# Performance work log

Hardware: AMD Instinct MI355X
Metric: run time of the kernel (lower is better)

## Reference

```python
import jax, jax.numpy as jnp
import numpy as np
from jax.scipy.linalg import solve_triangular

B, T, D = 4, 8192, 1024
HEAD_DIM = 128
CHUNK = 64


def setup_inputs() -> dict:
    key = jax.random.key(0)
    ks = jax.random.split(key, 8)
    H = D // HEAD_DIM
    x = jax.random.normal(ks[0], (B, T, D), dtype=jnp.float32)
    W_write = jax.random.normal(ks[1], (D, D), dtype=jnp.float32) * 0.02
    W_gate = jax.random.normal(ks[2], (H, D), dtype=jnp.float32) * 0.02
    W_out = jax.random.normal(ks[3], (D, D), dtype=jnp.float32) * 0.02
    W_beta = jax.random.normal(ks[4], (H, D), dtype=jnp.float32) * 0.02
    W_alpha = jax.random.normal(ks[5], (H, D), dtype=jnp.float32) * 0.02
    # dt_bias init as in torch: dt ~ loguniform(1e-3, 1e-1), bias = dt + log(-expm1(-dt))
    u = jax.random.uniform(ks[6], (H,), dtype=jnp.float32)
    dt = jnp.exp(u * (jnp.log(jnp.float32(0.1)) - jnp.log(jnp.float32(0.001))) + jnp.log(jnp.float32(0.001)))
    dt_bias = dt + jnp.log(-jnp.expm1(-dt))
    A_log = jnp.log(jax.random.uniform(ks[7], (H,), dtype=jnp.float32, minval=1e-3, maxval=16.0))
    return {"x": x, "W_write": W_write, "W_gate": W_gate, "W_out": W_out,
            "W_beta": W_beta, "W_alpha": W_alpha, "dt_bias": dt_bias, "A_log": A_log}


def reference(x, W_write, W_gate, W_out, W_beta, W_alpha, dt_bias, A_log):
    Bn, Tn, Dm = x.shape
    H = A_log.shape[0]
    d = Dm // H
    C = CHUNK
    assert Tn % C == 0
    N = Tn // C

    xf = x.astype(jnp.float32)
    v = (xf @ W_write.T).reshape(Bn, Tn, H, d)                       # write values
    gate = jax.nn.sigmoid(xf @ W_gate.T)[..., None]                  # (B,T,H,1)
    beta = jax.nn.sigmoid(xf @ W_beta.T)                             # (B,T,H)
    decay = -jnp.exp(A_log) * jax.nn.softplus(xf @ W_alpha.T + dt_bias)  # (B,T,H)

    rk = xf.reshape(Bn, Tn, H, d)
    rk = rk / jnp.maximum(jnp.linalg.norm(rk, axis=-1, keepdims=True), 1e-12)
    wk = jnp.pad(rk[:, :-1], ((0, 0), (1, 0), (0, 0), (0, 0)))       # token-shifted write key

    # (B,H,T,d)
    rk = rk.transpose(0, 2, 1, 3)
    wk = wk.transpose(0, 2, 1, 3)
    v = v.transpose(0, 2, 1, 3)
    bt = beta.transpose(0, 2, 1)[..., None]
    v = v * bt
    wk_beta = wk * bt

    # chunked: (B,H,N,C,d)
    rk = rk.reshape(Bn, H, N, C, d)
    wk = wk.reshape(Bn, H, N, C, d)
    v = v.reshape(Bn, H, N, C, d)
    wk_beta = wk_beta.reshape(Bn, H, N, C, d)
    dec = jnp.cumsum(decay.transpose(0, 2, 1).reshape(Bn, H, N, C), axis=-1)  # cumulative log-decay
    dec_exp = jnp.exp(dec)[..., None]

    lower = jnp.tril(jnp.ones((C, C), dtype=bool))            # incl. diagonal
    strict_lower = jnp.tril(jnp.ones((C, C), dtype=bool), -1)
    diff = dec[..., :, None] - dec[..., None, :]
    L_mask = jnp.exp(jnp.where(lower, diff, -jnp.inf))        # (B,H,N,C,C), 0 above diag

    # UT transform: torch's in-place row loop computes (I + M_strict)^{-1}
    M = jnp.einsum('bhnid,bhnjd->bhnij', wk_beta, wk) * L_mask
    M = jnp.where(strict_lower, M, jnp.float32(0.0))
    eye = jnp.eye(C, dtype=jnp.float32)
    A = solve_triangular(eye + M, jnp.broadcast_to(eye, M.shape), lower=True)

    v = A @ v
    wk_cumdecay = A @ (wk_beta * dec_exp)

    # sequential inter-chunk recurrence over N chunks, carrying matrix state S
    xs = (rk.transpose(2, 0, 1, 3, 4), wk.transpose(2, 0, 1, 3, 4), v.transpose(2, 0, 1, 3, 4),
          wk_cumdecay.transpose(2, 0, 1, 3, 4), dec.transpose(2, 0, 1, 3), L_mask.transpose(2, 0, 1, 3, 4))
    S0 = jnp.zeros((Bn, H, d, d), dtype=jnp.float32)

    def step(S, inp):
        rk_i, wk_i, v_i, wkcd_i, dec_i, L_i = inp
        attn = jnp.einsum('bhid,bhjd->bhij', rk_i, wk_i) * L_i
        attn = jnp.where(lower, attn, jnp.float32(0.0))
        v_new = v_i - wkcd_i @ S
        o_i = (rk_i * jnp.exp(dec_i)[..., None]) @ S + attn @ v_new
        dw = jnp.exp(dec_i[..., -1:] - dec_i)[..., None]                  # (B,H,C,1)
        S_new = S * jnp.exp(dec_i[..., -1])[..., None, None] + jnp.einsum('bhcd,bhce->bhde', wk_i * dw, v_new)
        return S_new, o_i

    _, o = jax.lax.scan(step, S0, xs)                 # (N,B,H,C,d)
    o = o.transpose(1, 2, 0, 3, 4).reshape(Bn, H, Tn, d).transpose(0, 2, 1, 3)  # (B,T,H,d)
    o = (o * gate).reshape(Bn, Tn, Dm)
    return (x + (o @ W_out.T)).astype(x.dtype)
```

## Files before the change

### kernel.cpp

```cpp
#include <hip/hip_runtime.h>
#include <math.h>

#define B_ 4
#define T_ 8192
#define D_ 1024
#define H_ 8
#define HD_ 128
#define C_ 64
#define N_ 128
#define BT_ (B_*T_)
#define BH_ (B_*H_)

typedef unsigned short ushort_t;
typedef unsigned long long ull_t;
typedef short s8v __attribute__((ext_vector_type(8)));
typedef float f32x4 __attribute__((ext_vector_type(4)));

__device__ __forceinline__ void fma4(float4& a, float s, const float4& v) {
  a.x += s*v.x; a.y += s*v.y; a.z += s*v.z; a.w += s*v.w;
}
__device__ __forceinline__ float bfu(unsigned int u16) {
  return __uint_as_float(u16 << 16);
}
__device__ __forceinline__ ushort_t f2bf(float f) {
  unsigned int x = __float_as_uint(f);
  x += 0x7FFFu + ((x >> 16) & 1u);
  return (ushort_t)(x >> 16);
}
__device__ __forceinline__ ull_t pack4bf(float a, float b, float c, float d) {
  return (ull_t)f2bf(a) | ((ull_t)f2bf(b) << 16) | ((ull_t)f2bf(c) << 32) | ((ull_t)f2bf(d) << 48);
}

__global__ __launch_bounds__(256) void k1_proj(
    const float* __restrict__ x, const float* __restrict__ Wg,
    const float* __restrict__ Wb, const float* __restrict__ Wa,
    const float* __restrict__ dt_bias, const float* __restrict__ A_log,
    float* __restrict__ gate_buf, float* __restrict__ beta_buf,
    float* __restrict__ decay_buf, float* __restrict__ innorm_buf) {
  const int row = blockIdx.x;
  const int b = row / T_, t = row % T_;
  const int tid = threadIdx.x;
  __shared__ float xs[D_];
  __shared__ float red[3][H_][4];
  __shared__ float scal[3][H_];
  __shared__ float rnorm[H_];

  ((float4*)xs)[tid] = ((const float4*)(x + (size_t)row * D_))[tid];
  __syncthreads();

  float pg[H_], pb[H_], pa[H_];
  #pragma unroll
  for (int h = 0; h < H_; h++) { pg[h] = 0.f; pb[h] = 0.f; pa[h] = 0.f; }
  for (int i = tid; i < D_; i += 256) {
    float xv = xs[i];
    #pragma unroll
    for (int h = 0; h < H_; h++) {
      pg[h] += xv * Wg[h*D_ + i];
      pb[h] += xv * Wb[h*D_ + i];
      pa[h] += xv * Wa[h*D_ + i];
    }
  }
  const int lane = tid & 63, wv = tid >> 6;
  #pragma unroll
  for (int h = 0; h < H_; h++) {
    float g = pg[h], bb = pb[h], aa = pa[h];
    #pragma unroll
    for (int off = 32; off > 0; off >>= 1) {
      g  += __shfl_down(g, off);
      bb += __shfl_down(bb, off);
      aa += __shfl_down(aa, off);
    }
    if (lane == 0) { red[0][h][wv] = g; red[1][h][wv] = bb; red[2][h][wv] = aa; }
  }
  float pn;
  {
    int hh = tid >> 5, e0 = (tid & 31) * 4;
    const float* xh = xs + hh*HD_ + e0;
    pn = xh[0]*xh[0] + xh[1]*xh[1] + xh[2]*xh[2] + xh[3]*xh[3];
  }
  #pragma unroll
  for (int off = 16; off > 0; off >>= 1) pn += __shfl_down(pn, off, 32);
  __syncthreads();
  if ((tid & 31) == 0) rnorm[tid >> 5] = fmaxf(sqrtf(pn), 1e-12f);
  if (tid < 24) {
    int p = tid >> 3, h = tid & 7;
    scal[p][h] = red[p][h][0] + red[p][h][1] + red[p][h][2] + red[p][h][3];
  }
  __syncthreads();
  if (tid < H_) {
    int h = tid;
    float g  = 1.f / (1.f + expf(-scal[0][h]));
    float be = 1.f / (1.f + expf(-scal[1][h]));
    float z  = scal[2][h] + dt_bias[h];
    float sp = (z > 20.f) ? z : log1pf(expf(z));
    float dc = -expf(A_log[h]) * sp;
    size_t idx = (size_t)(b*H_ + h)*T_ + t;
    gate_buf[idx] = g; beta_buf[idx] = be; decay_buf[idx] = dc;
    innorm_buf[idx] = 1.f / rnorm[h];
  }
}

__global__ __launch_bounds__(256) void k_gemm_bf16(
    const float* __restrict__ A, const float* __restrict__ W,
    const float* __restrict__ R, float* __restrict__ C,
    int M, int N, int K) {
  __shared__ ushort_t La[128*40];
  __shared__ ushort_t Lw[128*40];
  const int tid = threadIdx.x;
  const int w = tid >> 6, lane = tid & 63;
  const int l15 = lane & 15, l4 = lane >> 4;
  const int wr = w >> 1, wc = w & 1;

  const int nwg = gridDim.x;
  const int NB = N >> 7;
  const int bid = blockIdx.x;
  const int swz = (bid & 7) * (nwg >> 3) + (bid >> 3);
  const int row0 = (swz / NB) * 128, col0 = (swz % NB) * 128;

  f32x4 acc[4][4];
  #pragma unroll
  for (int m = 0; m < 4; m++)
    #pragma unroll
    for (int n = 0; n < 4; n++)
      #pragma unroll
      for (int r = 0; r < 4; r++) acc[m][n][r] = 0.f;

  float4 pa[2][2], pw[2][2];
  auto LOAD = [&](int k0) {
    #pragma unroll
    for (int s = 0; s < 2; s++) {
      int slot = tid + s*256;
      int rw = slot >> 2, kg = (slot & 3) * 8;
      const float* ap = A + (size_t)(row0 + rw)*K + k0 + kg;
      pa[s][0] = *(const float4*)ap; pa[s][1] = *(const float4*)(ap + 4);
      const float* wp = W + (size_t)(col0 + rw)*K + k0 + kg;
      pw[s][0] = *(const float4*)wp; pw[s][1] = *(const float4*)(wp + 4);
    }
  };

  LOAD(0);
  for (int k0 = 0; k0 < K; k0 += 32) {
    #pragma unroll
    for (int s = 0; s < 2; s++) {
      int slot = tid + s*256;
      int rw = slot >> 2, kg = (slot & 3) * 8;
      int4 ua, uw;
      ua.x = (int)f2bf(pa[s][0].x) | ((int)f2bf(pa[s][0].y) << 16);
      ua.y = (int)f2bf(pa[s][0].z) | ((int)f2bf(pa[s][0].w) << 16);
      ua.z = (int)f2bf(pa[s][1].x) | ((int)f2bf(pa[s][1].y) << 16);
      ua.w = (int)f2bf(pa[s][1].z) | ((int)f2bf(pa[s][1].w) << 16);
      uw.x = (int)f2bf(pw[s][0].x) | ((int)f2bf(pw[s][0].y) << 16);
      uw.y = (int)f2bf(pw[s][0].z) | ((int)f2bf(pw[s][0].w) << 16);
      uw.z = (int)f2bf(pw[s][1].x) | ((int)f2bf(pw[s][1].y) << 16);
      uw.w = (int)f2bf(pw[s][1].z) | ((int)f2bf(pw[s][1].w) << 16);
      *(int4*)&La[rw*40 + kg] = ua;
      *(int4*)&Lw[rw*40 + kg] = uw;
    }
    __syncthreads();
    if (k0 + 32 < K) LOAD(k0 + 32);
    s8v af[4], bf[4];
    #pragma unroll
    for (int m = 0; m < 4; m++)
      af[m] = *(const s8v*)&La[(wr*64 + m*16 + l15)*40 + l4*8];
    #pragma unroll
    for (int n = 0; n < 4; n++)
      bf[n] = *(const s8v*)&Lw[(wc*64 + n*16 + l15)*40 + l4*8];
    #pragma unroll
    for (int m = 0; m < 4; m++)
      #pragma unroll
      for (int n = 0; n < 4; n++)
        acc[m][n] = __builtin_amdgcn_mfma_f32_16x16x32_bf16(af[m], bf[n], acc[m][n], 0, 0, 0);
    __syncthreads();
  }

  #pragma unroll
  for (int m = 0; m < 4; m++) {
    #pragma unroll
    for (int r = 0; r < 4; r++) {
      int row = row0 + wr*64 + m*16 + l4*4 + r;
      size_t base = (size_t)row * N + col0 + wc*64 + l15;
      #pragma unroll
      for (int n = 0; n < 4; n++) {
        float v = acc[m][n][r];
        if (R) v += R[base + n*16];
        C[base + n*16] = v;
      }
    }
  }
}

__global__ __launch_bounds__(256) void k3_chunk(
    const float* __restrict__ x, float* __restrict__ v_io,
    const float* __restrict__ beta_buf, const float* __restrict__ decay_buf,
    const float* __restrict__ innorm_buf,
    ushort_t* __restrict__ wkcd_buf, ushort_t* __restrict__ attn_buf,
    float* __restrict__ dec_buf) {
  const int blk = blockIdx.x;
  const int bh = blk >> 7, n = blk & 127;
  const int b = bh >> 3, h = bh & 7;
  const int t0 = n * C_;
  const int tid = threadIdx.x;
  __shared__ float Pool[65*132];
  __shared__ float U[C_][66];
  __shared__ float dec[C_], beta_s[C_], edec[C_], inn[65];

  if (tid < 65) {
    int tg = t0 - 1 + tid;
    inn[tid] = (tg >= 0) ? innorm_buf[(size_t)bh*T_ + tg] : 0.f;
  }
  if (tid >= 192) {
    int i = tid - 192;
    size_t g = (size_t)bh*T_ + t0 + i;
    beta_s[i] = beta_buf[g];
    dec[i] = decay_buf[g];
  }
  __syncthreads();
  for (int idx = tid; idx < 65*32; idx += 256) {
    int i = idx >> 5, e4 = (idx & 31) * 4;
    int tg = t0 - 1 + i;
    float4 v = {0.f,0.f,0.f,0.f};
    if (tg >= 0) {
      v = *(const float4*)&x[((size_t)b*T_ + tg)*D_ + h*HD_ + e4];
      float s = inn[i];
      v.x*=s; v.y*=s; v.z*=s; v.w*=s;
    }
    *(float4*)&Pool[i*132 + e4] = v;
  }
  __syncthreads();
  if (tid == 0) { float s = 0.f; for (int i = 0; i < C_; i++) { s += dec[i]; dec[i] = s; } }
  __syncthreads();
  if (tid < C_) {
    edec[tid] = expf(dec[tid]);
    dec_buf[(size_t)bh*T_ + t0 + tid] = dec[tid];
  }
  const int bi = tid >> 4, bj = tid & 15;
  const int i0m = bi*4, j0m = bj*4;
  if (bi >= bj) {
    float m[4][4] = {{0.f}}, am[4][4] = {{0.f}};
    for (int k = 0; k < HD_; k += 4) {
      float4 wb[4];
      #pragma unroll
      for (int c = 0; c < 4; c++) wb[c] = *(const float4*)&Pool[(j0m+c)*132 + k];
      #pragma unroll
      for (int r = 0; r < 4; r++) {
        float4 wa = *(const float4*)&Pool[(i0m+r)*132 + k];
        float4 ra = *(const float4*)&Pool[(i0m+1+r)*132 + k];
        #pragma unroll
        for (int c = 0; c < 4; c++) {
          m[r][c]  += wa.x*wb[c].x + wa.y*wb[c].y + wa.z*wb[c].z + wa.w*wb[c].w;
          am[r][c] += ra.x*wb[c].x + ra.y*wb[c].y + ra.z*wb[c].z + ra.w*wb[c].w;
        }
      }
    }
    #pragma unroll
    for (int r = 0; r < 4; r++) {
      int i = i0m + r;
      #pragma unroll
      for (int c = 0; c < 4; c++) {
        int j = j0m + c;
        if (j < i) U[i][j] = m[r][c] * beta_s[i] * expf(dec[i]-dec[j]);
      }
      float a0 = (j0m+0 <= i) ? am[r][0]*expf(dec[i]-dec[j0m+0]) : 0.f;
      float a1 = (j0m+1 <= i) ? am[r][1]*expf(dec[i]-dec[j0m+1]) : 0.f;
      float a2 = (j0m+2 <= i) ? am[r][2]*expf(dec[i]-dec[j0m+2]) : 0.f;
      float a3 = (j0m+3 <= i) ? am[r][3]*expf(dec[i]-dec[j0m+3]) : 0.f;
      *(ull_t*)&attn_buf[(((size_t)bh*N_ + n)*C_ + i)*C_ + j0m] = pack4bf(a0,a1,a2,a3);
    }
  } else {
    #pragma unroll
    for (int r = 0; r < 4; r++) {
      int i = i0m + r;
      *(ull_t*)&attn_buf[(((size_t)bh*N_ + n)*C_ + i)*C_ + j0m] = 0ull;
    }
  }
  __syncthreads();
  if (tid < C_) {
    int j = tid;
    U[j][j] = 1.f;
    for (int i = j + 1; i < C_; i++) {
      float s = 0.f;
      for (int l = j; l < i; l++) s += U[i][l] * U[j][l];
      U[j][i] = -s;
    }
  }
  __syncthreads();
  for (int idx = tid; idx < C_*32; idx += 256) {
    int i = idx >> 5, e4 = (idx & 31) * 4;
    float s = beta_s[i] * edec[i];
    float4 v = *(const float4*)&Pool[i*132 + e4];
    v.x*=s; v.y*=s; v.z*=s; v.w*=s;
    *(float4*)&Pool[i*132 + e4] = v;
  }
  __syncthreads();
  const int i0 = (tid >> 4) * 4, e0 = (tid & 15) * 8;
  {
    float acc[4][8];
    #pragma unroll
    for (int r = 0; r < 4; r++)
      #pragma unroll
      for (int c = 0; c < 8; c++) acc[r][c] = 0.f;
    for (int j = 0; j < i0; j++) {
      float a0=U[j][i0], a1=U[j][i0+1], a2=U[j][i0+2], a3=U[j][i0+3];
      float4 w0 = *(const float4*)&Pool[j*132 + e0];
      float4 w1 = *(const float4*)&Pool[j*132 + e0 + 4];
      float ww[8] = {w0.x,w0.y,w0.z,w0.w,w1.x,w1.y,w1.z,w1.w};
      float aa[4] = {a0,a1,a2,a3};
      #pragma unroll
      for (int r = 0; r < 4; r++)
        #pragma unroll
        for (int c = 0; c < 8; c++) acc[r][c] += aa[r]*ww[c];
    }
    #pragma unroll
    for (int jj = 0; jj < 4; jj++) {
      int j = i0 + jj;
      float4 w0 = *(const float4*)&Pool[j*132 + e0];
      float4 w1 = *(const float4*)&Pool[j*132 + e0 + 4];
      float ww[8] = {w0.x,w0.y,w0.z,w0.w,w1.x,w1.y,w1.z,w1.w};
      for (int r = jj; r < 4; r++) {
        float a = U[j][i0+r];
        #pragma unroll
        for (int c = 0; c < 8; c++) acc[r][c] += a*ww[c];
      }
    }
    #pragma unroll
    for (int r = 0; r < 4; r++) {
      size_t base = ((size_t)bh*T_ + t0 + i0 + r)*HD_ + e0;
      *(ull_t*)&wkcd_buf[base]   = pack4bf(acc[r][0],acc[r][1],acc[r][2],acc[r][3]);
      *(ull_t*)&wkcd_buf[base+4] = pack4bf(acc[r][4],acc[r][5],acc[r][6],acc[r][7]);
    }
  }
  __syncthreads();
  for (int idx = tid; idx < C_*32; idx += 256) {
    int i = idx >> 5, e4 = (idx & 31) * 4;
    float4 v = *(const float4*)&v_io[((size_t)b*T_ + t0 + i)*D_ + h*HD_ + e4];
    float s = beta_s[i];
    v.x*=s; v.y*=s; v.z*=s; v.w*=s;
    *(float4*)&Pool[i*128 + e4] = v;
  }
  __syncthreads();
  {
    float acc[4][8];
    #pragma unroll
    for (int r = 0; r < 4; r++)
      #pragma unroll
      for (int c = 0; c < 8; c++) acc[r][c] = 0.f;
    for (int j = 0; j < i0; j++) {
      float aa[4] = {U[j][i0], U[j][i0+1], U[j][i0+2], U[j][i0+3]};
      float4 v0 = *(const float4*)&Pool[j*128 + e0];
      float4 v1 = *(const float4*)&Pool[j*128 + e0 + 4];
      float vv[8] = {v0.x,v0.y,v0.z,v0.w,v1.x,v1.y,v1.z,v1.w};
      #pragma unroll
      for (int r = 0; r < 4; r++)
        #pragma unroll
        for (int c = 0; c < 8; c++) acc[r][c] += aa[r]*vv[c];
    }
    #pragma unroll
    for (int jj = 0; jj < 4; jj++) {
      int j = i0 + jj;
      float4 v0 = *(const float4*)&Pool[j*128 + e0];
      float4 v1 = *(const float4*)&Pool[j*128 + e0 + 4];
      float vv[8] = {v0.x,v0.y,v0.z,v0.w,v1.x,v1.y,v1.z,v1.w};
      for (int r = jj; r < 4; r++) {
        float a = U[j][i0+r];
        #pragma unroll
        for (int c = 0; c < 8; c++) acc[r][c] += a*vv[c];
      }
    }
    #pragma unroll
    for (int r = 0; r < 4; r++) {
      size_t base = ((size_t)b*T_ + t0 + i0 + r)*D_ + h*HD_ + e0;
      float4 v0 = {acc[r][0],acc[r][1],acc[r][2],acc[r][3]};
      float4 v1 = {acc[r][4],acc[r][5],acc[r][6],acc[r][7]};
      *(float4*)&v_io[base]     = v0;
      *(float4*)&v_io[base + 4] = v1;
    }
  }
}

__global__ __launch_bounds__(512, 2) void k4_mfma(
    const float* __restrict__ x, float* __restrict__ v_io,
    const ushort_t* __restrict__ wkcd_buf, const ushort_t* __restrict__ attn_buf,
    const float* __restrict__ dec_buf, const float* __restrict__ gate_buf,
    const float* __restrict__ innorm_buf) {
  const int bid = blockIdx.x;
  const int xcd = bid & 7, jj = bid >> 3;
  const int bh = xcd*4 + (jj >> 3);
  const int eq = jj & 7;
  const int e0b = eq * 16;
  const int b = bh >> 3, h = bh & 7;
  const int tid = threadIdx.x;
  const int w = tid >> 6, lane = tid & 63;
  const int l15 = lane & 15, l4 = lane >> 4;
  const bool lowg = (w < 4);
  const int mw = w & 3;

  __shared__ ushort_t Krm[64*136];
  __shared__ ushort_t Wn [64*136];
  __shared__ ushort_t At [64*72];
  __shared__ ushort_t Sth[16*136];
  __shared__ ushort_t Stl[16*136];
  __shared__ ushort_t Vt [16*72];
  __shared__ float dec_s[64], gate_s[64], sc_s[64], dwn_s[64];

  f32x4 Sacc;
  Sacc[0]=0.f; Sacc[1]=0.f; Sacc[2]=0.f; Sacc[3]=0.f;

  float4 kf[4], wf[2], af;
  auto PF = [&](int nn) {
    const int t0n = nn * C_;
    #pragma unroll
    for (int k = 0; k < 4; k++) {
      int slot = tid + 512*k;
      int row = slot >> 5, q = slot & 31;
      kf[k] = *(const float4*)&x[((size_t)b*T_ + t0n + row)*D_ + h*HD_ + q*4];
    }
    #pragma unroll
    for (int k = 0; k < 2; k++) {
      int p = tid + 512*k;
      int row = p >> 4, cg = p & 15;
      wf[k] = *(const float4*)&wkcd_buf[((size_t)bh*T_ + t0n + row)*HD_ + cg*8];
    }
    af = *(const float4*)&attn_buf[(((size_t)bh*N_ + nn)*C_ + (tid>>3))*C_ + (tid&7)*8];
  };

  PF(0);

  for (int n = 0; n < N_; n++) {
    const int t0 = n * C_;
    #pragma unroll
    for (int k = 0; k < 4; k++) {
      int slot = tid + 512*k;
      int row = slot >> 5, q = slot & 31;
      float4 v = kf[k];
      *(ull_t*)&Krm[row*136 + q*4] = pack4bf(v.x, v.y, v.z, v.w);
    }
    #pragma unroll
    for (int k = 0; k < 2; k++) {
      int p = tid + 512*k;
      int row = p >> 4, cg = p & 15;
      int4 u = *(int4*)&wf[k];
      u.x ^= 0x80008000; u.y ^= 0x80008000; u.z ^= 0x80008000; u.w ^= 0x80008000;
      *(int4*)&Wn[row*136 + cg*8] = u;
    }
    *(int4*)&At[(tid>>3)*72 + (tid&7)*8] = *(int4*)&af;
    {
      ull_t ph = 0, pl = 0;
      #pragma unroll
      for (int r = 0; r < 4; r++) {
        float s = Sacc[r];
        ushort_t hb = f2bf(s);
        ushort_t lb = f2bf(s - bfu(hb));
        ph |= (ull_t)hb << (16*r);
        pl |= (ull_t)lb << (16*r);
      }
      *(ull_t*)&Sth[l15*136 + w*16 + l4*4] = ph;
      *(ull_t*)&Stl[l15*136 + w*16 + l4*4] = pl;
    }
    float vpf[4] = {0.f, 0.f, 0.f, 0.f};
    if (lowg) {
      #pragma unroll
      for (int r = 0; r < 4; r++)
        vpf[r] = v_io[((size_t)b*T_ + t0 + mw*16 + l4*4 + r)*D_ + h*HD_ + e0b + l15];
    }
    float ktf[16];
    #pragma unroll
    for (int ks = 0; ks < 2; ks++)
      #pragma unroll
      for (int j2 = 0; j2 < 8; j2++) {
        int tg = t0 - 1 + ks*32 + l4*8 + j2;
        ktf[ks*8+j2] = (tg >= 0)
            ? x[((size_t)b*T_ + tg)*D_ + h*HD_ + w*16 + l15] : 0.f;
      }
    float ipr = 0.f, icr = 0.f;
    if (tid < 64) {
      size_t g = (size_t)bh*T_ + t0 + tid;
      dec_s[tid]  = dec_buf[g];
      gate_s[tid] = gate_buf[g];
      icr = innorm_buf[g];
      ipr = (t0 - 1 + tid >= 0) ? innorm_buf[g - 1] : 0.f;
    }
    __syncthreads();
    if (tid < 64) {
      float dv = dec_s[tid], d63 = dec_s[63];
      sc_s[tid]  = expf(dv) * icr;
      dwn_s[tid] = expf(d63 - dv) * ipr;
    }
    if (n + 1 < N_) PF(n + 1);
    f32x4 oacc;
    if (lowg) {
      f32x4 acc;
      acc[0]=vpf[0]; acc[1]=vpf[1]; acc[2]=vpf[2]; acc[3]=vpf[3];
      #pragma unroll
      for (int ks = 0; ks < 4; ks++) {
        s8v a  = *(const s8v*)&Wn [(mw*16 + l15)*136 + ks*32 + l4*8];
        s8v sh = *(const s8v*)&Sth[l15*136 + ks*32 + l4*8];
        s8v sl = *(const s8v*)&Stl[l15*136 + ks*32 + l4*8];
        acc = __builtin_amdgcn_mfma_f32_16x16x32_bf16(a, sh, acc, 0, 0, 0);
        acc = __builtin_amdgcn_mfma_f32_16x16x32_bf16(a, sl, acc, 0, 0, 0);
      }
      ull_t pv = 0;
      #pragma unroll
      for (int r = 0; r < 4; r++) pv |= (ull_t)f2bf(acc[r]) << (16*r);
      *(ull_t*)&Vt[l15*72 + mw*16 + l4*4] = pv;
    } else {
      oacc[0]=0.f; oacc[1]=0.f; oacc[2]=0.f; oacc[3]=0.f;
      #pragma unroll
      for (int ks = 0; ks < 4; ks++) {
        s8v a  = *(const s8v*)&Krm[(mw*16 + l15)*136 + ks*32 + l4*8];
        s8v sh = *(const s8v*)&Sth[l15*136 + ks*32 + l4*8];
        s8v sl = *(const s8v*)&Stl[l15*136 + ks*32 + l4*8];
        oacc = __builtin_amdgcn_mfma_f32_16x16x32_bf16(a, sh, oacc, 0, 0, 0);
        oacc = __builtin_amdgcn_mfma_f32_16x16x32_bf16(a, sl, oacc, 0, 0, 0);
      }
    }
    __syncthreads();
    if (!lowg) {
      #pragma unroll
      for (int r = 0; r < 4; r++) oacc[r] *= sc_s[mw*16 + l4*4 + r];
      #pragma unroll
      for (int ks = 0; ks < 2; ks++) {
        s8v a  = *(const s8v*)&At[(mw*16 + l15)*72 + ks*32 + l4*8];
        s8v bv = *(const s8v*)&Vt[l15*72 + ks*32 + l4*8];
        oacc = __builtin_amdgcn_mfma_f32_16x16x32_bf16(a, bv, oacc, 0, 0, 0);
      }
      #pragma unroll
      for (int r = 0; r < 4; r++) {
        float g = gate_s[mw*16 + l4*4 + r];
        v_io[((size_t)b*T_ + t0 + mw*16 + l4*4 + r)*D_ + h*HD_ + e0b + l15] = oacc[r] * g;
      }
    }
    {
      float el = expf(dec_s[63]);
      #pragma unroll
      for (int r = 0; r < 4; r++) Sacc[r] *= el;
      #pragma unroll
      for (int ks = 0; ks < 2; ks++) {
        s8v am;
        #pragma unroll
        for (int j2 = 0; j2 < 8; j2++)
          am[j2] = (short)f2bf(ktf[ks*8+j2] * dwn_s[ks*32 + l4*8 + j2]);
        s8v bv = *(const s8v*)&Vt[l15*72 + ks*32 + l4*8];
        Sacc = __builtin_amdgcn_mfma_f32_16x16x32_bf16(am, bv, Sacc, 0, 0, 0);
      }
    }
    __syncthreads();
  }
}

extern "C" void kernel_launch(void* const* d_in, const int* in_sizes, int n_in,
                              void* d_out, int out_size, void* d_ws, size_t ws_size,
                              hipStream_t stream) {
  const float* x       = (const float*)d_in[0];
  const float* W_write = (const float*)d_in[1];
  const float* W_gate  = (const float*)d_in[2];
  const float* W_out   = (const float*)d_in[3];
  const float* W_beta  = (const float*)d_in[4];
  const float* W_alpha = (const float*)d_in[5];
  const float* dt_bias = (const float*)d_in[6];
  const float* A_log   = (const float*)d_in[7];
  float* out = (float*)d_out;

  const size_t SZ_BIG   = (size_t)BT_ * D_;
  const size_t SZ_ATTN  = (size_t)BH_ * N_ * C_ * C_;
  const size_t SZ_SMALL = (size_t)BH_ * T_;

  float*    vraw = (float*)d_ws;
  ushort_t* wkcd = (ushort_t*)(vraw + SZ_BIG);
  ushort_t* attn = wkcd + SZ_BIG;
  float*    decb = (float*)(attn + SZ_ATTN);
  float*    gateb  = decb + SZ_SMALL;
  float*    betab  = gateb + SZ_SMALL;
  float*    decayb = betab + SZ_SMALL;
  float*    innorm = decayb + SZ_SMALL;

  const int GEMM_GRID = (BT_/128) * (D_/128);

  k1_proj<<<BT_, 256, 0, stream>>>(x, W_gate, W_beta, W_alpha, dt_bias, A_log,
                                   gateb, betab, decayb, innorm);
  k_gemm_bf16<<<GEMM_GRID, 256, 0, stream>>>(x, W_write, nullptr, vraw,
                                             BT_, D_, D_);
  k3_chunk<<<BH_*N_, 256, 0, stream>>>(x, vraw, betab, decayb, innorm,
                                       wkcd, attn, decb);
  k4_mfma<<<BH_*8, 512, 0, stream>>>(x, vraw, wkcd, attn, decb, gateb, innorm);
  k_gemm_bf16<<<GEMM_GRID, 256, 0, stream>>>(vraw, W_out, x, out,
                                             BT_, D_, D_);
}
```

Baseline: 1.487 ms.

## Move chunk-level Gram and triangular-apply matmuls in k3 onto bf16 MFMA

Rewrites the per-chunk kernel so that the key Gram matrix and the two products of the inverted triangular matrix (with scaled keys and with values) run as 16x16x32 bf16 MFMA ops instead of scalar FP32 loops. The cumulative decay sum becomes a wavefront shuffle scan instead of a single-thread serial loop. Keys are staged in LDS as bf16, and values are split into hi/lo bf16 pairs to keep v precision close to FP32. This cuts the FP32 ALU work and serial steps in k3, but lowers the precision of the Gram matrix and wkcd. It also adds transposed LDS staging and scalar strided global loads.

```diff
diff --git a/kernel.cpp b/kernel.cpp
--- a/kernel.cpp
+++ b/kernel.cpp
@@ -16,9 +16,6 @@
 typedef short s8v __attribute__((ext_vector_type(8)));
 typedef float f32x4 __attribute__((ext_vector_type(4)));
 
-__device__ __forceinline__ void fma4(float4& a, float s, const float4& v) {
-  a.x += s*v.x; a.y += s*v.y; a.z += s*v.z; a.w += s*v.w;
-}
 __device__ __forceinline__ float bfu(unsigned int u16) {
   return __uint_as_float(u16 << 16);
 }
@@ -200,10 +197,31 @@
   const int b = bh >> 3, h = bh & 7;
   const int t0 = n * C_;
   const int tid = threadIdx.x;
-  __shared__ float Pool[65*132];
-  __shared__ float U[C_][66];
-  __shared__ float dec[C_], beta_s[C_], edec[C_], inn[65];
-
+  const int w = tid >> 6, lane = tid & 63;
+  const int l15 = lane & 15, l4 = lane >> 4;
+
+  __shared__ __align__(16) ushort_t R1[128*72];
+  __shared__ __align__(16) float    Gs[64*72];
+  __shared__ __align__(16) float    U[C_][74];
+  __shared__ __align__(16) ushort_t At[64*72];
+  __shared__ float dec_s[C_], beta_s[C_], inn[65], sbw[C_];
+  ushort_t* Ke   = R1;
+  ushort_t* WsT  = R1;
+  ushort_t* VbTh = (ushort_t*)Gs;
+  ushort_t* VbTl = (ushort_t*)&U[0][0];
+
+  float4 kf[9];
+  #pragma unroll
+  for (int k = 0; k < 9; k++) {
+    int slot = tid + 256*k;
+    float4 v = {0.f,0.f,0.f,0.f};
+    if (slot < 2080) {
+      int row = slot >> 5, q = slot & 31;
+      int tg = t0 - 1 + row;
+      if (tg >= 0) v = *(const float4*)&x[((size_t)b*T_ + tg)*D_ + h*HD_ + q*4];
+    }
+    kf[k] = v;
+  }
   if (tid < 65) {
     int tg = t0 - 1 + tid;
     inn[tid] = (tg >= 0) ? innorm_buf[(size_t)bh*T_ + tg] : 0.f;
@@ -212,68 +230,59 @@
     int i = tid - 192;
     size_t g = (size_t)bh*T_ + t0 + i;
     beta_s[i] = beta_buf[g];
-    dec[i] = decay_buf[g];
-  }
-  __syncthreads();
-  for (int idx = tid; idx < 65*32; idx += 256) {
-    int i = idx >> 5, e4 = (idx & 31) * 4;
-    int tg = t0 - 1 + i;
-    float4 v = {0.f,0.f,0.f,0.f};
-    if (tg >= 0) {
-      v = *(const float4*)&x[((size_t)b*T_ + tg)*D_ + h*HD_ + e4];
-      float s = inn[i];
-      v.x*=s; v.y*=s; v.z*=s; v.w*=s;
-    }
-    *(float4*)&Pool[i*132 + e4] = v;
-  }
-  __syncthreads();
-  if (tid == 0) { float s = 0.f; for (int i = 0; i < C_; i++) { s += dec[i]; dec[i] = s; } }
-  __syncthreads();
+    dec_s[i] = decay_buf[g];
+  }
+  __syncthreads();
+
   if (tid < C_) {
-    edec[tid] = expf(dec[tid]);
-    dec_buf[(size_t)bh*T_ + t0 + tid] = dec[tid];
-  }
-  const int bi = tid >> 4, bj = tid & 15;
-  const int i0m = bi*4, j0m = bj*4;
-  if (bi >= bj) {
-    float m[4][4] = {{0.f}}, am[4][4] = {{0.f}};
-    for (int k = 0; k < HD_; k += 4) {
-      float4 wb[4];
-      #pragma unroll
-      for (int c = 0; c < 4; c++) wb[c] = *(const float4*)&Pool[(j0m+c)*132 + k];
-      #pragma unroll
-      for (int r = 0; r < 4; r++) {
-        float4 wa = *(const float4*)&Pool[(i0m+r)*132 + k];
-        float4 ra = *(const float4*)&Pool[(i0m+1+r)*132 + k];
-        #pragma unroll
-        for (int c = 0; c < 4; c++) {
-          m[r][c]  += wa.x*wb[c].x + wa.y*wb[c].y + wa.z*wb[c].z + wa.w*wb[c].w;
-          am[r][c] += ra.x*wb[c].x + ra.y*wb[c].y + ra.z*wb[c].z + ra.w*wb[c].w;
-        }
-      }
-    }
-    #pragma unroll
-    for (int r = 0; r < 4; r++) {
-      int i = i0m + r;
-      #pragma unroll
-      for (int c = 0; c < 4; c++) {
-        int j = j0m + c;
-        if (j < i) U[i][j] = m[r][c] * beta_s[i] * expf(dec[i]-dec[j]);
-      }
-      float a0 = (j0m+0 <= i) ? am[r][0]*expf(dec[i]-dec[j0m+0]) : 0.f;
-      float a1 = (j0m+1 <= i) ? am[r][1]*expf(dec[i]-dec[j0m+1]) : 0.f;
-      float a2 = (j0m+2 <= i) ? am[r][2]*expf(dec[i]-dec[j0m+2]) : 0.f;
-      float a3 = (j0m+3 <= i) ? am[r][3]*expf(dec[i]-dec[j0m+3]) : 0.f;
-      *(ull_t*)&attn_buf[(((size_t)bh*N_ + n)*C_ + i)*C_ + j0m] = pack4bf(a0,a1,a2,a3);
-    }
-  } else {
-    #pragma unroll
-    for (int r = 0; r < 4; r++) {
-      int i = i0m + r;
-      *(ull_t*)&attn_buf[(((size_t)bh*N_ + n)*C_ + i)*C_ + j0m] = 0ull;
-    }
-  }
-  __syncthreads();
+    float v = dec_s[tid];
+    #pragma unroll
+    for (int off = 1; off < 64; off <<= 1) {
+      float p = __shfl_up(v, off);
+      if (tid >= off) v += p;
+    }
+    dec_s[tid] = v;
+    sbw[tid] = inn[tid] * beta_s[tid] * expf(v);
+    dec_buf[(size_t)bh*T_ + t0 + tid] = v;
+  }
+  #pragma unroll
+  for (int k = 0; k < 9; k++) {
+    int slot = tid + 256*k;
+    if (slot < 2080) {
+      int row = slot >> 5, q = slot & 31;
+      float s = inn[row];
+      float4 v = kf[k];
+      *(ull_t*)&Ke[row*136 + q*4] = pack4bf(v.x*s, v.y*s, v.z*s, v.w*s);
+    }
+  }
+  __syncthreads();
+
+  #pragma unroll
+  for (int tj = 0; tj < 4; tj++) {
+    f32x4 acc; acc[0]=0.f; acc[1]=0.f; acc[2]=0.f; acc[3]=0.f;
+    #pragma unroll
+    for (int ks = 0; ks < 4; ks++) {
+      s8v a  = *(const s8v*)&Ke[(w*16 + l15 + 1)*136 + ks*32 + l4*8];
+      s8v bv = *(const s8v*)&Ke[(tj*16 + l15)*136 + ks*32 + l4*8];
+      acc = __builtin_amdgcn_mfma_f32_16x16x32_bf16(a, bv, acc, 0, 0, 0);
+    }
+    #pragma unroll
+    for (int r = 0; r < 4; r++)
+      Gs[(w*16 + l4*4 + r)*72 + tj*16 + l15] = acc[r];
+  }
+  __syncthreads();
+
+  #pragma unroll
+  for (int k = 0; k < 16; k++) {
+    int idx = tid + 256*k;
+    int i = idx >> 6, j = idx & 63;
+    float ed = expf(dec_s[i] - dec_s[j]);
+    float g2 = Gs[i*72 + j];
+    attn_buf[(((size_t)bh*N_ + n)*C_ + i)*C_ + j] = (j <= i) ? f2bf(g2*ed) : (ushort_t)0;
+    if (j < i) U[i][j] = Gs[(i-1)*72 + j] * beta_s[i] * ed;
+  }
+  __syncthreads();
+
   if (tid < C_) {
     int j = tid;
     U[j][j] = 1.f;
@@ -284,95 +293,72 @@
     }
   }
   __syncthreads();
-  for (int idx = tid; idx < C_*32; idx += 256) {
-    int i = idx >> 5, e4 = (idx & 31) * 4;
-    float s = beta_s[i] * edec[i];
-    float4 v = *(const float4*)&Pool[i*132 + e4];
-    v.x*=s; v.y*=s; v.z*=s; v.w*=s;
-    *(float4*)&Pool[i*132 + e4] = v;
-  }
-  __syncthreads();
-  const int i0 = (tid >> 4) * 4, e0 = (tid & 15) * 8;
-  {
-    float acc[4][8];
-    #pragma unroll
-    for (int r = 0; r < 4; r++)
-      #pragma unroll
-      for (int c = 0; c < 8; c++) acc[r][c] = 0.f;
-    for (int j = 0; j < i0; j++) {
-      float a0=U[j][i0], a1=U[j][i0+1], a2=U[j][i0+2], a3=U[j][i0+3];
-      float4 w0 = *(const float4*)&Pool[j*132 + e0];
-      float4 w1 = *(const float4*)&Pool[j*132 + e0 + 4];
-      float ww[8] = {w0.x,w0.y,w0.z,w0.w,w1.x,w1.y,w1.z,w1.w};
-      float aa[4] = {a0,a1,a2,a3};
-      #pragma unroll
-      for (int r = 0; r < 4; r++)
-        #pragma unroll
-        for (int c = 0; c < 8; c++) acc[r][c] += aa[r]*ww[c];
-    }
-    #pragma unroll
-    for (int jj = 0; jj < 4; jj++) {
-      int j = i0 + jj;
-      float4 w0 = *(const float4*)&Pool[j*132 + e0];
-      float4 w1 = *(const float4*)&Pool[j*132 + e0 + 4];
-      float ww[8] = {w0.x,w0.y,w0.z,w0.w,w1.x,w1.y,w1.z,w1.w};
-      for (int r = jj; r < 4; r++) {
-        float a = U[j][i0+r];
-        #pragma unroll
-        for (int c = 0; c < 8; c++) acc[r][c] += a*ww[c];
-      }
+
+  #pragma unroll
+  for (int k = 0; k < 16; k++) {
+    int idx = tid + 256*k;
+    int i = idx >> 6, j = idx & 63;
+    At[i*72 + j] = (j <= i) ? f2bf(U[j][i]) : (ushort_t)0;
+  }
+  __syncthreads();
+
+  #pragma unroll
+  for (int k = 0; k < 8; k++) {
+    int slot = tid + 256*k;
+    int rg = slot >> 7, e = slot & 127;
+    float wv[4];
+    #pragma unroll
+    for (int c = 0; c < 4; c++) {
+      int j = rg*4 + c;
+      int tg = t0 - 1 + j;
+      wv[c] = (tg >= 0) ? x[((size_t)b*T_ + tg)*D_ + h*HD_ + e] * sbw[j] : 0.f;
+    }
+    *(ull_t*)&WsT[e*72 + rg*4] = pack4bf(wv[0], wv[1], wv[2], wv[3]);
+    ull_t ph = 0, pl = 0;
+    #pragma unroll
+    for (int c = 0; c < 4; c++) {
+      int j = rg*4 + c;
+      float vv = v_io[((size_t)b*T_ + t0 + j)*D_ + h*HD_ + e] * beta_s[j];
+      ushort_t hb = f2bf(vv);
+      ushort_t lb = f2bf(vv - bfu(hb));
+      ph |= (ull_t)hb << (16*c);
+      pl |= (ull_t)lb << (16*c);
+    }
+    *(ull_t*)&VbTh[e*72 + rg*4] = ph;
+    *(ull_t*)&VbTl[e*72 + rg*4] = pl;
+  }
+  __syncthreads();
+
+  #pragma unroll
+  for (int tj = 0; tj < 8; tj++) {
+    f32x4 acc; acc[0]=0.f; acc[1]=0.f; acc[2]=0.f; acc[3]=0.f;
+    #pragma unroll
+    for (int ks = 0; ks < 2; ks++) {
+      s8v a  = *(const s8v*)&At [(w*16 + l15)*72 + ks*32 + l4*8];
+      s8v bv = *(const s8v*)&WsT[(tj*16 + l15)*72 + ks*32 + l4*8];
+      acc = __builtin_amdgcn_mfma_f32_16x16x32_bf16(a, bv, acc, 0, 0, 0);
     }
     #pragma unroll
     for (int r = 0; r < 4; r++) {
-      size_t base = ((size_t)bh*T_ + t0 + i0 + r)*HD_ + e0;
-      *(ull_t*)&wkcd_buf[base]   = pack4bf(acc[r][0],acc[r][1],acc[r][2],acc[r][3]);
-      *(ull_t*)&wkcd_buf[base+4] = pack4bf(acc[r][4],acc[r][5],acc[r][6],acc[r][7]);
-    }
-  }
-  __syncthreads();
-  for (int idx = tid; idx < C_*32; idx += 256) {
-    int i = idx >> 5, e4 = (idx & 31) * 4;
-    float4 v = *(const float4*)&v_io[((size_t)b*T_ + t0 + i)*D_ + h*HD_ + e4];
-    float s = beta_s[i];
-    v.x*=s; v.y*=s; v.z*=s; v.w*=s;
-    *(float4*)&Pool[i*128 + e4] = v;
-  }
-  __syncthreads();
-  {
-    float acc[4][8];
-    #pragma unroll
-    for (int r = 0; r < 4; r++)
-      #pragma unroll
-      for (int c = 0; c < 8; c++) acc[r][c] = 0.f;
-    for (int j = 0; j < i0; j++) {
-      float aa[4] = {U[j][i0], U[j][i0+1], U[j][i0+2], U[j][i0+3]};
-      float4 v0 = *(const float4*)&Pool[j*128 + e0];
-      float4 v1 = *(const float4*)&Pool[j*128 + e0 + 4];
-      float vv[8] = {v0.x,v0.y,v0.z,v0.w,v1.x,v1.y,v1.z,v1.w};
-      #pragma unroll
-      for (int r = 0; r < 4; r++)
-        #pragma unroll
-        for (int c = 0; c < 8; c++) acc[r][c] += aa[r]*vv[c];
-    }
-    #pragma unroll
-    for (int jj = 0; jj < 4; jj++) {
-      int j = i0 + jj;
-      float4 v0 = *(const float4*)&Pool[j*128 + e0];
-      float4 v1 = *(const float4*)&Pool[j*128 + e0 + 4];
-      float vv[8] = {v0.x,v0.y,v0.z,v0.w,v1.x,v1.y,v1.z,v1.w};
-      for (int r = jj; r < 4; r++) {
-        float a = U[j][i0+r];
-        #pragma unroll
-        for (int c = 0; c < 8; c++) acc[r][c] += a*vv[c];
-      }
+      int i = w*16 + l4*4 + r, e = tj*16 + l15;
+      wkcd_buf[((size_t)bh*T_ + t0 + i)*HD_ + e] = f2bf(acc[r]);
+    }
+  }
+  #pragma unroll
+  for (int tj = 0; tj < 8; tj++) {
+    f32x4 acc; acc[0]=0.f; acc[1]=0.f; acc[2]=0.f; acc[3]=0.f;
+    #pragma unroll
+    for (int ks = 0; ks < 2; ks++) {
+      s8v a  = *(const s8v*)&At  [(w*16 + l15)*72 + ks*32 + l4*8];
+      s8v bh16 = *(const s8v*)&VbTh[(tj*16 + l15)*72 + ks*32 + l4*8];
+      s8v bl16 = *(const s8v*)&VbTl[(tj*16 + l15)*72 + ks*32 + l4*8];
+      acc = __builtin_amdgcn_mfma_f32_16x16x32_bf16(a, bh16, acc, 0, 0, 0);
+      acc = __builtin_amdgcn_mfma_f32_16x16x32_bf16(a, bl16, acc, 0, 0, 0);
     }
     #pragma unroll
     for (int r = 0; r < 4; r++) {
-      size_t base = ((size_t)b*T_ + t0 + i0 + r)*D_ + h*HD_ + e0;
-      float4 v0 = {acc[r][0],acc[r][1],acc[r][2],acc[r][3]};
-      float4 v1 = {acc[r][4],acc[r][5],acc[r][6],acc[r][7]};
-      *(float4*)&v_io[base]     = v0;
-      *(float4*)&v_io[base + 4] = v1;
+      int i = w*16 + l4*4 + r, e = tj*16 + l15;
+      v_io[((size_t)b*T_ + t0 + i)*D_ + h*HD_ + e] = acc[r];
     }
   }
 }
```

Result: no change. 1.476 ms (-0.7%).
